# Kernel optimization log

Hardware: AMD Instinct MI355X
Metric: run time of the kernel (lower is better)

The kernel has to match this reference:

```python
import jax, jax.numpy as jnp
import numpy as np

B, H, S, P = 4, 16, 1024, 64
D = H * P  # state_size = 1024


def setup_inputs() -> dict:
    key = jax.random.key(0)
    k0, k1, k2, k3, k4 = jax.random.split(key, 5)
    q = jax.random.normal(k0, (B * H, S, P), jnp.float32)
    k = jax.random.normal(k1, (B * H, S, P), jnp.float32)
    v = jax.random.normal(k2, (B * H, S, P), jnp.float32)
    # xavier_uniform for the merge projection (fan_in = fan_out = D)
    limit = np.sqrt(6.0 / (D + D)).astype(np.float32)
    w_merge = jax.random.uniform(k3, (D, D), jnp.float32, -limit, limit)
    # causal position mask: True = masked (as used by masked_fill)
    position_mask = jnp.triu(jnp.ones((S, S), dtype=bool), k=1)
    # source-length padding mask: True = padded position
    lengths = jax.random.randint(k4, (B,), S // 2, S + 1)
    src_length_mask = jnp.arange(S)[None, :] >= lengths[:, None]
    return {"q": q, "k": k, "v": v, "w_merge": w_merge,
            "position_mask": position_mask, "src_length_mask": src_length_mask}


def reference(q, k, v, w_merge, position_mask, src_length_mask):
    # q,k,v: [B*H, S, P]; position_mask: [S,S] bool; src_length_mask: [B,S] bool
    BH, T, Pp = q.shape
    nb = src_length_mask.shape[0]
    nh = BH // nb
    scale = 1.0 / np.sqrt(Pp).astype(np.float32)
    # logits = bmm(q, k^T) * scale
    logits = jnp.einsum('btp,bsp->bts', q, k) * scale  # [B*H, T, S]
    logits = logits.reshape(nb, nh, T, T)
    logits = jnp.where(position_mask[None, None, :, :], -jnp.inf, logits)
    logits = jnp.where(src_length_mask[:, None, None, :], -jnp.inf, logits)
    scores = jax.nn.softmax(logits, axis=-1).reshape(BH, T, T)
    # dropout is identity in eval / p=0
    data = jnp.einsum('bts,bsp->btp', scores, v)  # [B*H, T, P]
    # merge heads: [B, H, T, P] -> [B, T, H*P]
    data = data.reshape(nb, nh, T, Pp).transpose(0, 2, 1, 3).reshape(nb, T, nh * Pp)
    return data @ w_merge.T  # Linear(bias=False)
```

## Files before the change

kernel.cpp:

```cpp
#include <hip/hip_runtime.h>
#include <hip/hip_bf16.h>
#include <math.h>


typedef _Float16 f16x8 __attribute__((ext_vector_type(8)));
typedef unsigned short u16x8 __attribute__((ext_vector_type(8)));
typedef float f32x4 __attribute__((ext_vector_type(4)));

union H8 { u16x8 u; f16x8 h; };

static __device__ __forceinline__ unsigned short f2hu(float f) {
  _Float16 h = (_Float16)f;
  unsigned short u;
  __builtin_memcpy(&u, &h, 2);
  return u;
}

#define MFMA16(a, b, c) __builtin_amdgcn_mfma_f32_16x16x32_f16((a), (b), (c), 0, 0, 0)

static __device__ __forceinline__ void gload16(const void* g, void* l) {
  __builtin_amdgcn_global_load_lds(
      (const __attribute__((address_space(1))) unsigned int*)g,
      (__attribute__((address_space(3))) unsigned int*)l, 16, 0, 0);
}

__global__ __launch_bounds__(256) void prep_all(const float* __restrict__ w,
                                                const int* __restrict__ smask,
                                                const float* __restrict__ kin,
                                                const float* __restrict__ vin,
                                                unsigned short* __restrict__ w_h,
                                                unsigned short* __restrict__ k_sw,
                                                unsigned short* __restrict__ v_sw,
                                                int* __restrict__ lengths) {
  const int bid = blockIdx.x;
  const int tid = threadIdx.x;
  if (bid < 4) {
    __shared__ int sh[256];
    int4 m = ((const int4*)(smask + bid * 1024))[tid];
    sh[tid] = (m.x != 0) + (m.y != 0) + (m.z != 0) + (m.w != 0);
    __syncthreads();
    for (int o = 128; o > 0; o >>= 1) {
      if (tid < o) sh[tid] += sh[tid + o];
      __syncthreads();
    }
    if (tid == 0) lengths[bid] = 1024 - sh[0];
  } else if (bid < 1028) {
    int idx = (bid - 4) * 256 + tid;
    float4 f = ((const float4*)w)[idx];
    ushort4 o;
    o.x = f2hu(f.x); o.y = f2hu(f.y); o.z = f2hu(f.z); o.w = f2hu(f.w);
    ((ushort4*)w_h)[idx] = o;
  } else if (bid < 3076) {
    int idx = (bid - 1028) * 256 + tid;
    const float4* src = ((const float4*)kin) + (size_t)idx * 2;
    float4 a = src[0], b = src[1];
    u16x8 o;
    o[0] = f2hu(a.x); o[1] = f2hu(a.y); o[2] = f2hu(a.z); o[3] = f2hu(a.w);
    o[4] = f2hu(b.x); o[5] = f2hu(b.y); o[6] = f2hu(b.z); o[7] = f2hu(b.w);
    int bh = idx >> 13;
    int i = idx & 8191;
    int s = i >> 3;
    int c16 = i & 7;
    int kt = s >> 6, r = s & 63;
    int xb = (r * 128 + c16 * 16) ^ ((r & 7) << 4);
    *(u16x8*)((char*)k_sw + ((size_t)(bh * 16 + kt)) * 8192 + xb) = o;
  } else {
    const int t = bid - 3076;
    const int bh = t >> 4;
    const int st = t & 15;
    __shared__ unsigned short T[64][72];
    const float* vp = vin + ((size_t)bh * 1024 + st * 64) * 64;
#pragma unroll
    for (int i = 0; i < 4; ++i) {
      int e = i * 256 + tid;
      int row = e >> 4;
      int c4 = (e & 15) * 4;
      float4 f = *(const float4*)(vp + row * 64 + c4);
      T[c4 + 0][row] = f2hu(f.x);
      T[c4 + 1][row] = f2hu(f.y);
      T[c4 + 2][row] = f2hu(f.z);
      T[c4 + 3][row] = f2hu(f.w);
    }
    __syncthreads();
#pragma unroll
    for (int i = 0; i < 4; ++i) {
      int e = i * 256 + tid;
      int feat = e >> 4;
      int c4 = (e & 15) * 4;
      ushort4 o;
      o.x = T[feat][c4 + 0]; o.y = T[feat][c4 + 1];
      o.z = T[feat][c4 + 2]; o.w = T[feat][c4 + 3];
      int xb = (feat * 128 + c4 * 2) ^ ((feat & 7) << 4);
      *(ushort4*)((char*)v_sw + ((size_t)(bh * 16 + st)) * 8192 + xb) = o;
    }
  }
}

static __device__ __forceinline__ void qset_step(const unsigned short* Kcur,
                                                 const unsigned short* Vcur,
                                                 char* Pw, const H8 qa[2],
                                                 f32x4 (&oacc)[4], f32x4& sumacc,
                                                 int kt, int qbase, int len,
                                                 int l15, int kgrp, int wv) {
  f32x4 sacc[4] = {};
#pragma unroll
  for (int kb = 0; kb < 2; kb++)
#pragma unroll
    for (int nb = 0; nb < 4; nb++) {
      H8 bb;
      bb.u = *(const u16x8*)((const char*)Kcur +
              (((nb * 16 + l15) * 128 + (kb * 32 + kgrp * 8) * 2) ^ ((l15 & 7) << 4)));
      sacc[nb] = MFMA16(qa[kb].h, bb.h, sacc[nb]);
    }

#pragma unroll
  for (int nb = 0; nb < 4; nb++) {
    int scol = kt * 64 + nb * 16 + l15;
#pragma unroll
    for (int r = 0; r < 4; r++) {
      int trow = qbase + wv * 16 + kgrp * 4 + r;
      float pv = (scol > trow || scol >= len)
                     ? 0.f
                     : __expf(fmaf(sacc[nb][r], 0.125f, -5.0f));
      int prow = kgrp * 4 + r;
      int pcol = nb * 16 + l15;
      *(unsigned short*)(Pw + ((prow * 128 + pcol * 2) ^ ((prow & 7) << 4))) = f2hu(pv);
    }
  }

  const f16x8 ones_h = {(_Float16)1.f, (_Float16)1.f, (_Float16)1.f, (_Float16)1.f,
                        (_Float16)1.f, (_Float16)1.f, (_Float16)1.f, (_Float16)1.f};
#pragma unroll
  for (int kb = 0; kb < 2; kb++) {
    H8 pa;
    pa.u = *(const u16x8*)((const char*)Pw +
            ((l15 * 128 + (kb * 32 + kgrp * 8) * 2) ^ ((l15 & 7) << 4)));
    sumacc = MFMA16(pa.h, ones_h, sumacc);
#pragma unroll
    for (int nb = 0; nb < 4; nb++) {
      H8 vb;
      vb.u = *(const u16x8*)((const char*)Vcur +
              (((nb * 16 + l15) * 128 + (kb * 32 + kgrp * 8) * 2) ^ ((l15 & 7) << 4)));
      oacc[nb] = MFMA16(pa.h, vb.h, oacc[nb]);
    }
  }
}

__global__ __launch_bounds__(256, 2) void attn_pair(const float* __restrict__ q,
                                                    const unsigned short* __restrict__ k_sw,
                                                    const unsigned short* __restrict__ v_sw,
                                                    const int* __restrict__ lengths,
                                                    unsigned short* __restrict__ attn_out) {
  const int wg = blockIdx.x;
  const int idx = (wg & 7) * 64 + (wg >> 3);
  const int bh = idx >> 3;
  const int p = idx & 7;
  const int qtA = p;
  const int qtB = 15 - p;
  const int b = bh >> 4;
  const int h = bh & 15;
  const int tid = threadIdx.x;
  const int lane = tid & 63;
  const int wv = tid >> 6;
  const int l15 = lane & 15;
  const int kgrp = lane >> 4;
  const int qbaseA = qtA * 64;
  const int qbaseB = qtB * 64;
  const int len = lengths[b];

  __shared__ __align__(16) unsigned short Kb[2][4096];
  __shared__ __align__(16) unsigned short Vb[2][4096];
  __shared__ __align__(16) unsigned short Plds[4][2][1024];

  const char* kbase_sw = (const char*)k_sw + (size_t)bh * 16 * 8192;
  const char* vbase_sw = (const char*)v_sw + (size_t)bh * 16 * 8192;
  char* PwA = (char*)(&Plds[wv][0][0]);
  char* PwB = (char*)(&Plds[wv][1][0]);

  H8 qaA[2], qaB[2];
  {
    const float* qpA = q + ((size_t)bh * 1024 + qbaseA + wv * 16 + l15) * 64;
    const float* qpB = q + ((size_t)bh * 1024 + qbaseB + wv * 16 + l15) * 64;
#pragma unroll
    for (int kb = 0; kb < 2; kb++) {
      const float* a0 = qpA + kb * 32 + kgrp * 8;
      float4 f0 = *(const float4*)(a0);
      float4 f1 = *(const float4*)(a0 + 4);
      u16x8 u;
      u[0] = f2hu(f0.x); u[1] = f2hu(f0.y); u[2] = f2hu(f0.z); u[3] = f2hu(f0.w);
      u[4] = f2hu(f1.x); u[5] = f2hu(f1.y); u[6] = f2hu(f1.z); u[7] = f2hu(f1.w);
      qaA[kb].u = u;
      const float* b0 = qpB + kb * 32 + kgrp * 8;
      float4 g0 = *(const float4*)(b0);
      float4 g1 = *(const float4*)(b0 + 4);
      u16x8 v;
      v[0] = f2hu(g0.x); v[1] = f2hu(g0.y); v[2] = f2hu(g0.z); v[3] = f2hu(g0.w);
      v[4] = f2hu(g1.x); v[5] = f2hu(g1.y); v[6] = f2hu(g1.z); v[7] = f2hu(g1.w);
      qaB[kb].u = v;
    }
  }

  f32x4 oaccA[4] = {}, oaccB[4] = {};
  f32x4 sumA = {}, sumB = {};

  const int nktA = qtA + 1;
  const int capB = (len - 1 < qbaseB + 63) ? (len - 1) : (qbaseB + 63);
  const int nktB = (capB >> 6) + 1;

#pragma unroll
  for (int j = 0; j < 2; ++j) {
    int ch = wv * 2 + j;
    gload16(kbase_sw + ch * 1024 + lane * 16, (char*)Kb[0] + ch * 1024);
    gload16(vbase_sw + ch * 1024 + lane * 16, (char*)Vb[0] + ch * 1024);
  }
  asm volatile("s_waitcnt vmcnt(0)" ::: "memory");
  __builtin_amdgcn_s_barrier();

  for (int kt = 0; kt < nktB; ++kt) {
    const int cur = kt & 1;
    if (kt + 1 < nktB) {
      const char* ks = kbase_sw + (size_t)(kt + 1) * 8192;
      const char* vs = vbase_sw + (size_t)(kt + 1) * 8192;
#pragma unroll
      for (int j = 0; j < 2; ++j) {
        int ch = wv * 2 + j;
        gload16(ks + ch * 1024 + lane * 16, (char*)Kb[cur ^ 1] + ch * 1024);
        gload16(vs + ch * 1024 + lane * 16, (char*)Vb[cur ^ 1] + ch * 1024);
      }
    }

    qset_step(Kb[cur], Vb[cur], PwB, qaB, oaccB, sumB, kt, qbaseB, len, l15, kgrp, wv);
    if (kt < nktA)
      qset_step(Kb[cur], Vb[cur], PwA, qaA, oaccA, sumA, kt, qbaseA, len, l15, kgrp, wv);

    asm volatile("s_waitcnt vmcnt(0)" ::: "memory");
    __builtin_amdgcn_s_barrier();
  }

#pragma unroll
  for (int nb = 0; nb < 4; nb++)
#pragma unroll
    for (int r = 0; r < 4; r++) {
      int feat = nb * 16 + l15;
      int trowA = qbaseA + wv * 16 + kgrp * 4 + r;
      attn_out[((size_t)b * 1024 + trowA) * 1024 + h * 64 + feat] =
          f2hu(oaccA[nb][r] / sumA[r]);
      int trowB = qbaseB + wv * 16 + kgrp * 4 + r;
      attn_out[((size_t)b * 1024 + trowB) * 1024 + h * 64 + feat] =
          f2hu(oaccB[nb][r] / sumB[r]);
    }
}

__global__ __launch_bounds__(256) void merge_kernel(const unsigned short* __restrict__ a_h,
                                                    const unsigned short* __restrict__ w_h,
                                                    float* __restrict__ out) {
  const int n0 = blockIdx.x * 64;
  const int m0 = blockIdx.y * 64;
  const int tid = threadIdx.x;
  const int lane = tid & 63;
  const int wv = tid >> 6;
  const int l15 = lane & 15;
  const int kgrp = lane >> 4;

  __shared__ unsigned short Alds[64 * 64];
  __shared__ unsigned short Wlds[64 * 64];

  f32x4 acc[4] = {};

  for (int kt = 0; kt < 16; ++kt) {
    __syncthreads();
#pragma unroll
    for (int i = 0; i < 4; i++) {
      int e = i * 256 + tid;
      int row = e >> 4;
      int c4 = (e & 15) * 4;
      ushort4 av = *(const ushort4*)(a_h + (size_t)(m0 + row) * 1024 + kt * 64 + c4);
      *(ushort4*)((char*)Alds + ((row * 128 + c4 * 2) ^ ((row & 7) << 4))) = av;
      ushort4 wv4 = *(const ushort4*)(w_h + (size_t)(n0 + row) * 1024 + kt * 64 + c4);
      *(ushort4*)((char*)Wlds + ((row * 128 + c4 * 2) ^ ((row & 7) << 4))) = wv4;
    }
    __syncthreads();
#pragma unroll
    for (int kb = 0; kb < 2; kb++) {
      int arow = wv * 16 + l15;
      H8 aa;
      aa.u = *(const u16x8*)((const char*)Alds +
                             ((arow * 128 + (kb * 32 + kgrp * 8) * 2) ^ ((arow & 7) << 4)));
#pragma unroll
      for (int nb = 0; nb < 4; nb++) {
        int wrow = nb * 16 + l15;
        H8 bb;
        bb.u = *(const u16x8*)((const char*)Wlds +
                               ((wrow * 128 + (kb * 32 + kgrp * 8) * 2) ^ ((wrow & 7) << 4)));
        acc[nb] = MFMA16(aa.h, bb.h, acc[nb]);
      }
    }
  }
#pragma unroll
  for (int nb = 0; nb < 4; nb++)
#pragma unroll
    for (int r = 0; r < 4; r++)
      out[(size_t)(m0 + wv * 16 + kgrp * 4 + r) * 1024 + n0 + nb * 16 + l15] = acc[nb][r];
}

extern "C" void kernel_launch(void* const* d_in, const int* in_sizes, int n_in,
                              void* d_out, int out_size, void* d_ws, size_t ws_size,
                              hipStream_t stream) {
  const float* q = (const float*)d_in[0];
  const float* k = (const float*)d_in[1];
  const float* v = (const float*)d_in[2];
  const float* w = (const float*)d_in[3];
  const int* smask = (const int*)d_in[5];
  float* out = (float*)d_out;

  char* ws = (char*)d_ws;
  const size_t MB = 1024 * 1024;
  int* lengths = (int*)ws;
  unsigned short* w_h = (unsigned short*)(ws + 256);
  unsigned short* attn_h = (unsigned short*)(ws + 256 + 2 * MB);
  unsigned short* k_sw = (unsigned short*)(ws + 256 + 10 * MB);
  unsigned short* v_sw = (unsigned short*)(ws + 256 + 18 * MB);

  hipLaunchKernelGGL(prep_all, dim3(4100), dim3(256), 0, stream,
                     w, smask, k, v, w_h, k_sw, v_sw, lengths);
  hipLaunchKernelGGL(attn_pair, dim3(512), dim3(256), 0, stream,
                     q, k_sw, v_sw, lengths, attn_h);
  hipLaunchKernelGGL(merge_kernel, dim3(16, 64), dim3(256), 0, stream, attn_h, w_h, out);
}
```

Baseline: 64.75 us.

## Triple-buffer K/V tiles with one barrier per step and MFMA priority hints

The attention kernel's K/V shared-memory staging goes from double to triple buffering. Loads are issued two tiles ahead, and each iteration waits with a partial vmcnt so the next tile's loads stay in flight. The trailing wait and barrier are folded into one wait and barrier at the top of each iteration. s_setprio hints are placed around the MFMA blocks to favour matrix issue over other waves. LDS use per block grows by 16KB, which could limit occupancy at two blocks per CU.

New measurement: 65.05 us. No clear change (+0.5%).

```diff
diff --git a/kernel.cpp b/kernel.cpp
--- a/kernel.cpp
+++ b/kernel.cpp
@@ -103,6 +103,7 @@
                                                  int kt, int qbase, int len,
                                                  int l15, int kgrp, int wv) {
   f32x4 sacc[4] = {};
+  __builtin_amdgcn_s_setprio(1);
 #pragma unroll
   for (int kb = 0; kb < 2; kb++)
 #pragma unroll
@@ -112,6 +113,7 @@
               (((nb * 16 + l15) * 128 + (kb * 32 + kgrp * 8) * 2) ^ ((l15 & 7) << 4)));
       sacc[nb] = MFMA16(qa[kb].h, bb.h, sacc[nb]);
     }
+  __builtin_amdgcn_s_setprio(0);
 
 #pragma unroll
   for (int nb = 0; nb < 4; nb++) {
@@ -130,6 +132,7 @@
 
   const f16x8 ones_h = {(_Float16)1.f, (_Float16)1.f, (_Float16)1.f, (_Float16)1.f,
                         (_Float16)1.f, (_Float16)1.f, (_Float16)1.f, (_Float16)1.f};
+  __builtin_amdgcn_s_setprio(1);
 #pragma unroll
   for (int kb = 0; kb < 2; kb++) {
     H8 pa;
@@ -144,6 +147,7 @@
       oacc[nb] = MFMA16(pa.h, vb.h, oacc[nb]);
     }
   }
+  __builtin_amdgcn_s_setprio(0);
 }
 
 __global__ __launch_bounds__(256, 2) void attn_pair(const float* __restrict__ q,
@@ -168,8 +172,8 @@
   const int qbaseB = qtB * 64;
   const int len = lengths[b];
 
-  __shared__ __align__(16) unsigned short Kb[2][4096];
-  __shared__ __align__(16) unsigned short Vb[2][4096];
+  __shared__ __align__(16) unsigned short Kb[3][4096];
+  __shared__ __align__(16) unsigned short Vb[3][4096];
   __shared__ __align__(16) unsigned short Plds[4][2][1024];
 
   const char* kbase_sw = (const char*)k_sw + (size_t)bh * 16 * 8192;
@@ -193,10 +197,10 @@
       const float* b0 = qpB + kb * 32 + kgrp * 8;
       float4 g0 = *(const float4*)(b0);
       float4 g1 = *(const float4*)(b0 + 4);
-      u16x8 v;
-      v[0] = f2hu(g0.x); v[1] = f2hu(g0.y); v[2] = f2hu(g0.z); v[3] = f2hu(g0.w);
-      v[4] = f2hu(g1.x); v[5] = f2hu(g1.y); v[6] = f2hu(g1.z); v[7] = f2hu(g1.w);
-      qaB[kb].u = v;
+      u16x8 vv;
+      vv[0] = f2hu(g0.x); vv[1] = f2hu(g0.y); vv[2] = f2hu(g0.z); vv[3] = f2hu(g0.w);
+      vv[4] = f2hu(g1.x); vv[5] = f2hu(g1.y); vv[6] = f2hu(g1.z); vv[7] = f2hu(g1.w);
+      qaB[kb].u = vv;
     }
   }
 
@@ -207,35 +211,38 @@
   const int capB = (len - 1 < qbaseB + 63) ? (len - 1) : (qbaseB + 63);
   const int nktB = (capB >> 6) + 1;
 
-#pragma unroll
-  for (int j = 0; j < 2; ++j) {
-    int ch = wv * 2 + j;
-    gload16(kbase_sw + ch * 1024 + lane * 16, (char*)Kb[0] + ch * 1024);
-    gload16(vbase_sw + ch * 1024 + lane * 16, (char*)Vb[0] + ch * 1024);
-  }
-  asm volatile("s_waitcnt vmcnt(0)" ::: "memory");
-  __builtin_amdgcn_s_barrier();
+#define STAGE_T(t, buf)                                                      \
+  do {                                                                       \
+    const char* ks_ = kbase_sw + (size_t)(t) * 8192;                         \
+    const char* vs_ = vbase_sw + (size_t)(t) * 8192;                         \
+    _Pragma("unroll") for (int j = 0; j < 2; ++j) {                          \
+      int ch = wv * 2 + j;                                                   \
+      gload16(ks_ + ch * 1024 + lane * 16, (char*)Kb[buf] + ch * 1024);      \
+      gload16(vs_ + ch * 1024 + lane * 16, (char*)Vb[buf] + ch * 1024);      \
+    }                                                                        \
+  } while (0)
+
+  STAGE_T(0, 0);
+  STAGE_T(1, 1);
 
   for (int kt = 0; kt < nktB; ++kt) {
-    const int cur = kt & 1;
+    const int cur = kt % 3;
     if (kt + 1 < nktB) {
-      const char* ks = kbase_sw + (size_t)(kt + 1) * 8192;
-      const char* vs = vbase_sw + (size_t)(kt + 1) * 8192;
-#pragma unroll
-      for (int j = 0; j < 2; ++j) {
-        int ch = wv * 2 + j;
-        gload16(ks + ch * 1024 + lane * 16, (char*)Kb[cur ^ 1] + ch * 1024);
-        gload16(vs + ch * 1024 + lane * 16, (char*)Vb[cur ^ 1] + ch * 1024);
-      }
+      asm volatile("s_waitcnt vmcnt(4)" ::: "memory");
+    } else {
+      asm volatile("s_waitcnt vmcnt(0)" ::: "memory");
+    }
+    __builtin_amdgcn_s_barrier();
+    if (kt + 2 < nktB) {
+      const int nbuf = (kt + 2) % 3;
+      STAGE_T(kt + 2, nbuf);
     }
 
     qset_step(Kb[cur], Vb[cur], PwB, qaB, oaccB, sumB, kt, qbaseB, len, l15, kgrp, wv);
     if (kt < nktA)
       qset_step(Kb[cur], Vb[cur], PwA, qaA, oaccA, sumA, kt, qbaseA, len, l15, kgrp, wv);
-
-    asm volatile("s_waitcnt vmcnt(0)" ::: "memory");
-    __builtin_amdgcn_s_barrier();
-  }
+  }
+#undef STAGE_T
 
 #pragma unroll
   for (int nb = 0; nb < 4; nb++)
```
